# Optimization experiments

Hardware: AMD Instinct MI355X
Metric: run time of the kernel (lower is better)

Reference implementation:

```python
import jax, jax.numpy as jnp
import numpy as np

EPS = 1e-12  # torch F.normalize default eps

def _l1_normalize(x):
    # x / max(||x||_1, eps) along last dim
    n = jnp.sum(jnp.abs(x), axis=-1, keepdims=True)
    return x / jnp.maximum(n, EPS)

def setup_inputs() -> dict:
    key = jax.random.key(0)
    k1, k2, k3, k4 = jax.random.split(key, 4)
    N, D, E, R = 100000, 128, 500000, 500
    z = jax.random.normal(k1, (N, D), dtype=jnp.float32)
    edge_index = jax.random.randint(k2, (2, E), 0, N, dtype=jnp.int64)
    edge_type = jax.random.randint(k3, (E,), 0, R, dtype=jnp.int64)
    rel_emb = jax.random.normal(k4, (R, D), dtype=jnp.float32)
    # match TransE init: L2-normalized relation embeddings
    rel_emb = rel_emb / jnp.linalg.norm(rel_emb, axis=-1, keepdims=True)
    return {"z": z, "edge_index": edge_index, "edge_type": edge_type, "rel_emb": rel_emb}

def reference(z, edge_index, edge_type, rel_emb):
    head = _l1_normalize(z[edge_index[0]])   # [E, D]
    tail = _l1_normalize(z[edge_index[1]])   # [E, D]
    rel = rel_emb[edge_type]                  # [E, D]
    return -jnp.sum(jnp.abs(head + rel - tail), axis=-1)  # [E]
```

## Files before the change

### kernel.cpp

```cpp
#include <hip/hip_runtime.h>
#include <hip/hip_fp16.h>

#define D 128
#define EPS 1e-12f
#define FP8_SCALE 64.0f
#define FP8_INV_SCALE 0.015625f

typedef float v2f __attribute__((ext_vector_type(2)));


__global__ void normalize_to_fp8_kernel(const float* __restrict__ z,
                                        unsigned char* __restrict__ zn, int N) {
    int wave_in_block = threadIdx.x >> 6;
    int lane = threadIdx.x & 63;
    int row = blockIdx.x * (blockDim.x >> 6) + wave_in_block;
    if (row >= N) return;
    const float2* zp = (const float2*)(z + (size_t)row * D);
    float2 v = zp[lane];
    float s = fabsf(v.x) + fabsf(v.y);
    #pragma unroll
    for (int m = 32; m >= 1; m >>= 1)
        s += __shfl_xor(s, m, 64);
    float f = FP8_SCALE / fmaxf(s, EPS);
    int p = __builtin_amdgcn_cvt_pk_fp8_f32(v.x * f, v.y * f, 0, false);
    unsigned short* rowp = (unsigned short*)(zn + (size_t)row * D);
    rowp[lane] = (unsigned short)(p & 0xffff);
}

__global__ void transe_score_fp8_kernel(const unsigned char* __restrict__ zn,
                                        const int* __restrict__ eidx,
                                        const int* __restrict__ etype,
                                        const float* __restrict__ rel,
                                        float* __restrict__ out, int E) {
    int gtid = blockIdx.x * blockDim.x + threadIdx.x;
    int e = gtid >> 3;
    int lane8 = threadIdx.x & 7;
    if (e >= E) return;

    int h = eidx[e];
    int t = eidx[E + e];
    int r = etype[e];

    uint4 hv = ((const uint4*)(zn + (size_t)h * D))[lane8];
    uint4 tv = ((const uint4*)(zn + (size_t)t * D))[lane8];
    const float4* rp = (const float4*)(rel + (size_t)r * D) + lane8 * 4;
    float4 r0 = rp[0], r1 = rp[1], r2 = rp[2], r3 = rp[3];
    float rf[16] = {r0.x, r0.y, r0.z, r0.w, r1.x, r1.y, r1.z, r1.w,
                    r2.x, r2.y, r2.z, r2.w, r3.x, r3.y, r3.z, r3.w};

    unsigned int hw[4] = {hv.x, hv.y, hv.z, hv.w};
    unsigned int tw[4] = {tv.x, tv.y, tv.z, tv.w};

    float s = 0.0f;
    #pragma unroll
    for (int k = 0; k < 4; ++k) {
        v2f h0 = __builtin_amdgcn_cvt_pk_f32_fp8(hw[k], false);
        v2f h1 = __builtin_amdgcn_cvt_pk_f32_fp8(hw[k], true);
        v2f t0 = __builtin_amdgcn_cvt_pk_f32_fp8(tw[k], false);
        v2f t1 = __builtin_amdgcn_cvt_pk_f32_fp8(tw[k], true);
        s += fabsf(fmaf(h0.x - t0.x, FP8_INV_SCALE, rf[4 * k    ]));
        s += fabsf(fmaf(h0.y - t0.y, FP8_INV_SCALE, rf[4 * k + 1]));
        s += fabsf(fmaf(h1.x - t1.x, FP8_INV_SCALE, rf[4 * k + 2]));
        s += fabsf(fmaf(h1.y - t1.y, FP8_INV_SCALE, rf[4 * k + 3]));
    }
    s += __shfl_xor(s, 1, 64);
    s += __shfl_xor(s, 2, 64);
    s += __shfl_xor(s, 4, 64);
    if (lane8 == 0) out[e] = -s;
}


__global__ void normalize_to_half_kernel(const float* __restrict__ z,
                                         __half* __restrict__ zn, int N) {
    int wave_in_block = threadIdx.x >> 6;
    int lane = threadIdx.x & 63;
    int row = blockIdx.x * (blockDim.x >> 6) + wave_in_block;
    if (row >= N) return;
    const float2* zp = (const float2*)(z + (size_t)row * D);
    float2 v = zp[lane];
    float s = fabsf(v.x) + fabsf(v.y);
    #pragma unroll
    for (int m = 32; m >= 1; m >>= 1)
        s += __shfl_xor(s, m, 64);
    float inv = 1.0f / fmaxf(s, EPS);
    __half2* znp = (__half2*)(zn + (size_t)row * D);
    znp[lane] = __floats2half2_rn(v.x * inv, v.y * inv);
}

__global__ void transe_score_half_kernel(const __half* __restrict__ zn,
                                         const int* __restrict__ eidx,
                                         const int* __restrict__ etype,
                                         const float* __restrict__ rel,
                                         float* __restrict__ out, int E) {
    int gtid = blockIdx.x * blockDim.x + threadIdx.x;
    int e = gtid >> 4;
    int lane16 = threadIdx.x & 15;
    if (e >= E) return;

    int h = eidx[e];
    int t = eidx[E + e];
    int r = etype[e];

    float4 hraw = *(const float4*)(zn + (size_t)h * D + lane16 * 8);
    float4 traw = *(const float4*)(zn + (size_t)t * D + lane16 * 8);
    const float4* rp = (const float4*)(rel + (size_t)r * D) + lane16 * 2;
    float4 r0 = rp[0];
    float4 r1 = rp[1];

    const __half2* hh = (const __half2*)&hraw;
    const __half2* th = (const __half2*)&traw;
    float rf[8] = {r0.x, r0.y, r0.z, r0.w, r1.x, r1.y, r1.z, r1.w};

    float s = 0.0f;
    #pragma unroll
    for (int k = 0; k < 4; ++k) {
        float2 hf = __half22float2(hh[k]);
        float2 tf = __half22float2(th[k]);
        s += fabsf(hf.x + rf[2 * k]     - tf.x);
        s += fabsf(hf.y + rf[2 * k + 1] - tf.y);
    }
    s += __shfl_xor(s, 1, 64);
    s += __shfl_xor(s, 2, 64);
    s += __shfl_xor(s, 4, 64);
    s += __shfl_xor(s, 8, 64);
    if (lane16 == 0) out[e] = -s;
}

extern "C" void kernel_launch(void* const* d_in, const int* in_sizes, int n_in,
                              void* d_out, int out_size, void* d_ws, size_t ws_size,
                              hipStream_t stream) {
    const float* z    = (const float*)d_in[0];
    const int*   eidx = (const int*)d_in[1];
    const int*   etyp = (const int*)d_in[2];
    const float* rel  = (const float*)d_in[3];
    float* out = (float*)d_out;

    int N = in_sizes[0] / D;
    int E = in_sizes[2];

    size_t need_fp8 = (size_t)N * D;
    if (ws_size >= need_fp8) {
        unsigned char* zn = (unsigned char*)d_ws;
        int blocks1 = (N + 3) / 4;
        normalize_to_fp8_kernel<<<blocks1, 256, 0, stream>>>(z, zn, N);
        int blocks2 = (E + 31) / 32;
        transe_score_fp8_kernel<<<blocks2, 256, 0, stream>>>(zn, eidx, etyp, rel, out, E);
    } else {
        __half* zn = (__half*)d_ws;
        int blocks1 = (N + 3) / 4;
        normalize_to_half_kernel<<<blocks1, 256, 0, stream>>>(z, zn, N);
        int blocks2 = (E + 15) / 16;
        transe_score_half_kernel<<<blocks2, 256, 0, stream>>>(zn, eidx, etyp, rel, out, E);
    }
}
```

Baseline: 118.8 us.

## Convert relation table to fp16 in prep kernel and use nontemporal loads

The normalization kernel now also converts the relation embedding table to fp16, and processes two rows per wave with float4 loads. The scoring kernel reads fp16 relations instead of fp32, halving relation gather bytes, and uses nontemporal loads and stores for the streaming index and output arrays. This lowers memory traffic in the gather-heavy scoring pass at the cost of a small extra conversion step and some added rounding error in the relation values.

```diff
diff --git a/kernel.cpp b/kernel.cpp
--- a/kernel.cpp
+++ b/kernel.cpp
@@ -7,49 +7,67 @@
 #define FP8_INV_SCALE 0.015625f
 
 typedef float v2f __attribute__((ext_vector_type(2)));
+typedef float v4f __attribute__((ext_vector_type(4)));
 
 
-__global__ void normalize_to_fp8_kernel(const float* __restrict__ z,
-                                        unsigned char* __restrict__ zn, int N) {
-    int wave_in_block = threadIdx.x >> 6;
+__global__ void build_tables_kernel(const float* __restrict__ z,
+                                    const float* __restrict__ rel,
+                                    unsigned char* __restrict__ zn,
+                                    __half* __restrict__ relh,
+                                    int N, int R) {
+    int wave = threadIdx.x >> 6;
     int lane = threadIdx.x & 63;
-    int row = blockIdx.x * (blockDim.x >> 6) + wave_in_block;
-    if (row >= N) return;
-    const float2* zp = (const float2*)(z + (size_t)row * D);
-    float2 v = zp[lane];
-    float s = fabsf(v.x) + fabsf(v.y);
-    #pragma unroll
-    for (int m = 32; m >= 1; m >>= 1)
-        s += __shfl_xor(s, m, 64);
-    float f = FP8_SCALE / fmaxf(s, EPS);
-    int p = __builtin_amdgcn_cvt_pk_fp8_f32(v.x * f, v.y * f, 0, false);
-    unsigned short* rowp = (unsigned short*)(zn + (size_t)row * D);
-    rowp[lane] = (unsigned short)(p & 0xffff);
+    int rh   = lane >> 5;
+    int sub  = lane & 31;
+    int row  = blockIdx.x * ((blockDim.x >> 6) * 2) + wave * 2 + rh;
+
+    if (row < N) {
+        const v4f* zp = (const v4f*)(z + (size_t)row * D);
+        v4f v = __builtin_nontemporal_load(zp + sub);
+        float s = fabsf(v.x) + fabsf(v.y) + fabsf(v.z) + fabsf(v.w);
+        #pragma unroll
+        for (int m = 16; m >= 1; m >>= 1)
+            s += __shfl_xor(s, m, 64);
+        float f = FP8_SCALE / fmaxf(s, EPS);
+        unsigned int p = __builtin_amdgcn_cvt_pk_fp8_f32(v.x * f, v.y * f, 0, false);
+        p = __builtin_amdgcn_cvt_pk_fp8_f32(v.z * f, v.w * f, p, true);
+        ((unsigned int*)(zn + (size_t)row * D))[sub] = p;
+    } else {
+        int rr = row - N;
+        if (rr < R) {
+            const float4* rp = (const float4*)(rel + (size_t)rr * D);
+            float4 v = rp[sub];
+            float2 w;
+            ((__half2*)&w)[0] = __floats2half2_rn(v.x, v.y);
+            ((__half2*)&w)[1] = __floats2half2_rn(v.z, v.w);
+            ((float2*)(relh + (size_t)rr * D))[sub] = w;
+        }
+    }
 }
 
 __global__ void transe_score_fp8_kernel(const unsigned char* __restrict__ zn,
+                                        const __half* __restrict__ relh,
                                         const int* __restrict__ eidx,
                                         const int* __restrict__ etype,
-                                        const float* __restrict__ rel,
                                         float* __restrict__ out, int E) {
     int gtid = blockIdx.x * blockDim.x + threadIdx.x;
     int e = gtid >> 3;
     int lane8 = threadIdx.x & 7;
     if (e >= E) return;
 
-    int h = eidx[e];
-    int t = eidx[E + e];
-    int r = etype[e];
+    int h = __builtin_nontemporal_load(eidx + e);
+    int t = __builtin_nontemporal_load(eidx + E + e);
+    int r = __builtin_nontemporal_load(etype + e);
 
     uint4 hv = ((const uint4*)(zn + (size_t)h * D))[lane8];
     uint4 tv = ((const uint4*)(zn + (size_t)t * D))[lane8];
-    const float4* rp = (const float4*)(rel + (size_t)r * D) + lane8 * 4;
-    float4 r0 = rp[0], r1 = rp[1], r2 = rp[2], r3 = rp[3];
-    float rf[16] = {r0.x, r0.y, r0.z, r0.w, r1.x, r1.y, r1.z, r1.w,
-                    r2.x, r2.y, r2.z, r2.w, r3.x, r3.y, r3.z, r3.w};
+    const uint4* rp = (const uint4*)(relh + (size_t)r * D);
+    uint4 rv0 = rp[lane8 * 2];
+    uint4 rv1 = rp[lane8 * 2 + 1];
 
     unsigned int hw[4] = {hv.x, hv.y, hv.z, hv.w};
     unsigned int tw[4] = {tv.x, tv.y, tv.z, tv.w};
+    unsigned int rw[8] = {rv0.x, rv0.y, rv0.z, rv0.w, rv1.x, rv1.y, rv1.z, rv1.w};
 
     float s = 0.0f;
     #pragma unroll
@@ -58,15 +76,17 @@
         v2f h1 = __builtin_amdgcn_cvt_pk_f32_fp8(hw[k], true);
         v2f t0 = __builtin_amdgcn_cvt_pk_f32_fp8(tw[k], false);
         v2f t1 = __builtin_amdgcn_cvt_pk_f32_fp8(tw[k], true);
-        s += fabsf(fmaf(h0.x - t0.x, FP8_INV_SCALE, rf[4 * k    ]));
-        s += fabsf(fmaf(h0.y - t0.y, FP8_INV_SCALE, rf[4 * k + 1]));
-        s += fabsf(fmaf(h1.x - t1.x, FP8_INV_SCALE, rf[4 * k + 2]));
-        s += fabsf(fmaf(h1.y - t1.y, FP8_INV_SCALE, rf[4 * k + 3]));
+        float2 r0 = __half22float2(*(const __half2*)&rw[2 * k]);
+        float2 r1 = __half22float2(*(const __half2*)&rw[2 * k + 1]);
+        s += fabsf(fmaf(h0.x - t0.x, FP8_INV_SCALE, r0.x));
+        s += fabsf(fmaf(h0.y - t0.y, FP8_INV_SCALE, r0.y));
+        s += fabsf(fmaf(h1.x - t1.x, FP8_INV_SCALE, r1.x));
+        s += fabsf(fmaf(h1.y - t1.y, FP8_INV_SCALE, r1.y));
     }
     s += __shfl_xor(s, 1, 64);
     s += __shfl_xor(s, 2, 64);
     s += __shfl_xor(s, 4, 64);
-    if (lane8 == 0) out[e] = -s;
+    if (lane8 == 0) __builtin_nontemporal_store(-s, out + e);
 }
 
 
@@ -137,14 +157,21 @@
 
     int N = in_sizes[0] / D;
     int E = in_sizes[2];
+    int R = in_sizes[3] / D;
 
-    size_t need_fp8 = (size_t)N * D;
+    size_t zn_bytes   = (size_t)N * D;
+    size_t zn_aligned = (zn_bytes + 255) & ~(size_t)255;
+    size_t relh_bytes = (size_t)R * D * sizeof(__half);
+    size_t need_fp8   = zn_aligned + relh_bytes;
+
     if (ws_size >= need_fp8) {
         unsigned char* zn = (unsigned char*)d_ws;
-        int blocks1 = (N + 3) / 4;
-        normalize_to_fp8_kernel<<<blocks1, 256, 0, stream>>>(z, zn, N);
+        __half* relh = (__half*)((unsigned char*)d_ws + zn_aligned);
+        int rows = N + R;
+        int blocks1 = (rows + 7) / 8;
+        build_tables_kernel<<<blocks1, 256, 0, stream>>>(z, rel, zn, relh, N, R);
         int blocks2 = (E + 31) / 32;
-        transe_score_fp8_kernel<<<blocks2, 256, 0, stream>>>(zn, eidx, etyp, rel, out, E);
+        transe_score_fp8_kernel<<<blocks2, 256, 0, stream>>>(zn, relh, eidx, etyp, out, E);
     } else {
         __half* zn = (__half*)d_ws;
         int blocks1 = (N + 3) / 4;
```

Measured after the change: 115.6 us. -2.7%, faster.
